# Kernel tuning notes

Hardware: AMD Instinct MI355X
Metric: run time of the kernel (lower is better)

The kernel has to match this reference:

```python
import jax, jax.numpy as jnp
import numpy as np

S, B, H = 2048, 2, 4096
NH, NG, HD = 32, 2, 128        # query heads, kv groups, head dim
ROT = 64                        # rotary dims (half of head dim)


def apply_rope(x, rope):
    # x: [s, b, n, hd]; rope: [s, 1, rot//2, 2]
    s = x.shape[0]
    rot = rope.shape[-2] * 2
    xr, xp = x[..., :rot], x[..., rot:]
    xs = xr.reshape(xr.shape[:-1] + (rot // 2, 2))          # [s,b,n,rot/2,2]
    rc = rope[:s].reshape(s, 1, 1, rot // 2, 2)             # broadcast over b, n
    c, sn = rc[..., 0], rc[..., 1]
    x0, x1 = xs[..., 0], xs[..., 1]
    out = jnp.stack([x0 * c - x1 * sn, x1 * c + x0 * sn], axis=-1)
    return jnp.concatenate([out.reshape(xr.shape), xp], axis=-1)


def setup_inputs() -> dict:
    key = jax.random.key(0)
    k1, k2, k3, k4 = jax.random.split(key, 4)
    hidden_states = jax.random.normal(k1, (S, B, H), dtype=jnp.float32)
    # causal boolean mask: True = attend
    causal = jnp.tril(jnp.ones((S, S), dtype=bool))
    attention_mask = jnp.broadcast_to(causal[None, None], (B, 1, S, S))
    # standard RoPE cache: [s, 1, rot//2, 2] = (cos, sin)
    pos = jnp.arange(S, dtype=jnp.float32)
    inv_freq = 1.0 / (10000.0 ** (jnp.arange(0, ROT // 2, dtype=jnp.float32) / (ROT // 2)))
    ang = pos[:, None] * inv_freq[None, :]
    rotary_pos_emb = jnp.stack([jnp.cos(ang), jnp.sin(ang)], axis=-1)[:, None]
    W_qkv = jax.random.normal(k2, (NH * HD + 2 * NG * HD, H), dtype=jnp.float32) * (H ** -0.5)
    b_qkv = jax.random.normal(k3, (NH * HD + 2 * NG * HD,), dtype=jnp.float32) * 0.02
    W_dense = jax.random.normal(k4, (H, NH * HD), dtype=jnp.float32) * ((NH * HD) ** -0.5)
    return {"hidden_states": hidden_states, "attention_mask": attention_mask,
            "rotary_pos_emb": rotary_pos_emb, "W_qkv": W_qkv, "b_qkv": b_qkv,
            "W_dense": W_dense}


def reference(hidden_states, attention_mask, rotary_pos_emb, W_qkv, b_qkv, W_dense):
    s, b, _ = hidden_states.shape
    r = NH // NG  # query heads per kv group
    mixed = jnp.einsum('sbh,oh->sbo', hidden_states, W_qkv) + b_qkv
    q = mixed[..., :NH * HD].reshape(s, b, NH, HD)
    k = mixed[..., NH * HD:NH * HD + NG * HD].reshape(s, b, NG, HD)
    v = mixed[..., NH * HD + NG * HD:].reshape(s, b, NG, HD)
    q = apply_rope(q, rotary_pos_emb)
    k = apply_rope(k, rotary_pos_emb)
    # GQA: keep kv at NG heads, give q a [g, r] split instead of materializing repeats
    qg = q.reshape(s, b, NG, r, HD)
    scale = HD ** -0.5
    scores = jnp.einsum('sbgrd,tbgd->bgrst', qg, k) * scale     # [b,g,r,s,t]
    mask = attention_mask[:, :, None]                            # [b,1,1,s,t]
    scores = jnp.where(mask, scores, jnp.finfo(scores.dtype).min)
    probs = jax.nn.softmax(scores, axis=-1)
    ctx = jnp.einsum('bgrst,tbgd->sbgrd', probs, v)              # [s,b,g,r,d]
    ctx = ctx.reshape(s, b, NH * HD)
    out = jnp.einsum('sbp,hp->sbh', ctx, W_dense)
    return out
```

## Files before the change

kernel.cpp:

```cpp
#include <hip/hip_runtime.h>
#include <cstdint>
#include <cstddef>


#define S_LEN 2048
#define BATCH 2
#define NHEADS 32
#define NGROUPS 2
#define HEADDIM 128
#define OQKV 4608
#define KSTRIDE 160
#define VSTRIDE 2080

typedef __attribute__((ext_vector_type(4))) float f32x4;
typedef __attribute__((ext_vector_type(4))) unsigned int u32x4;
typedef __attribute__((ext_vector_type(8))) unsigned short u16x8;
typedef __attribute__((ext_vector_type(8))) short s16x8;

union B8 { u32x4 q; u16x8 u; s16x8 s; };

__device__ __forceinline__ unsigned short f2b(float f) {
  unsigned int u = __builtin_bit_cast(unsigned int, f);
  u += 0x7fffu + ((u >> 16) & 1u);
  return (unsigned short)(u >> 16);
}
__device__ __forceinline__ float b2f(unsigned short h) {
  unsigned int u = ((unsigned int)h) << 16;
  return __builtin_bit_cast(float, u);
}

__device__ __forceinline__ void gload16(const unsigned short* g, unsigned short* l) {
  __builtin_amdgcn_global_load_lds(
      (const __attribute__((address_space(1))) void*)g,
      (__attribute__((address_space(3))) void*)l, 16, 0, 0);
}

__global__ __launch_bounds__(256) void cvt_kernel(const float* __restrict__ in,
                                                  unsigned short* __restrict__ out) {
  size_t i = (size_t)blockIdx.x * 256 + threadIdx.x;
  const f32x4* p = (const f32x4*)(in + i * 8);
  f32x4 a = p[0], b = p[1];
  B8 r;
  r.u[0] = f2b(a[0]); r.u[1] = f2b(a[1]); r.u[2] = f2b(a[2]); r.u[3] = f2b(a[3]);
  r.u[4] = f2b(b[0]); r.u[5] = f2b(b[1]); r.u[6] = f2b(b[2]); r.u[7] = f2b(b[3]);
  *(u32x4*)(out + i * 8) = r.q;
}

template<int A_FP32, int HAS_BIAS, int OUT_BF16>
__global__ __launch_bounds__(256) void gemm_bt(const void* __restrict__ Ap,
                                               const unsigned short* __restrict__ Bt,
                                               const float* __restrict__ bias,
                                               void* __restrict__ Cp,
                                               int M, int N, int K) {
  __shared__ __align__(16) unsigned short lA[128 * 32];
  __shared__ __align__(16) unsigned short lB[128 * 32];
  const int tid = threadIdx.x;
  const int wave = tid >> 6, lane = tid & 63;
  const int quad = lane >> 4, l15 = lane & 15;
  const int nwg = gridDim.x * gridDim.y;
  int lin = blockIdx.y * gridDim.x + blockIdx.x;
  int swz = (lin & 7) * (nwg >> 3) + (lin >> 3);
  const int bx = swz % gridDim.x, by = swz / gridDim.x;
  const int m0 = by * 128, n0 = bx * 128;
  const int wm = (wave & 1) * 64, wn = (wave >> 1) * 64;
  const int grow = wave * 16 + (lane >> 2);
  const int gcol = (lane & 3) * 8;
  unsigned short* lAw = lA + wave * 512;
  unsigned short* lBw = lB + wave * 512;
  f32x4 acc[4][4] = {};
  const unsigned short* Ab = (const unsigned short*)Ap;
  const float* Af = (const float*)Ap;
  const int ar = tid >> 1, acf = (tid & 1) * 16;
  f32x4 x0, x1, x2, x3;
  if (A_FP32) {
    const f32x4* p = (const f32x4*)(Af + (size_t)(m0 + ar) * K + acf);
    x0 = p[0]; x1 = p[1]; x2 = p[2]; x3 = p[3];
  }
  for (int k0 = 0; k0 < K; k0 += 32) {
    __syncthreads();
    if (A_FP32) {
      B8 c0, c1;
      for (int e = 0; e < 4; ++e) {
        c0.u[e] = f2b(x0[e]); c0.u[e + 4] = f2b(x1[e]);
        c1.u[e] = f2b(x2[e]); c1.u[e + 4] = f2b(x3[e]);
      }
      *(u32x4*)(lA + ar * 32 + acf) = c0.q;
      *(u32x4*)(lA + ar * 32 + acf + 8) = c1.q;
    } else {
      gload16(Ab + (size_t)(m0 + grow) * K + k0 + gcol, lAw);
      gload16(Ab + (size_t)(m0 + 64 + grow) * K + k0 + gcol, lAw + 2048);
    }
    gload16(Bt + (size_t)(n0 + grow) * K + k0 + gcol, lBw);
    gload16(Bt + (size_t)(n0 + 64 + grow) * K + k0 + gcol, lBw + 2048);
    __syncthreads();
    if (A_FP32 && k0 + 32 < K) {
      const f32x4* p = (const f32x4*)(Af + (size_t)(m0 + ar) * K + k0 + 32 + acf);
      x0 = p[0]; x1 = p[1]; x2 = p[2]; x3 = p[3];
    }
    B8 af[4], bf[4];
    for (int i = 0; i < 4; ++i)
      af[i].q = *(const u32x4*)(lA + (wm + 16 * i + l15) * 32 + quad * 8);
    for (int j = 0; j < 4; ++j)
      bf[j].q = *(const u32x4*)(lB + (wn + 16 * j + l15) * 32 + quad * 8);
    for (int i = 0; i < 4; ++i)
      for (int j = 0; j < 4; ++j)
        acc[i][j] = __builtin_amdgcn_mfma_f32_16x16x32_bf16(af[i].s, bf[j].s, acc[i][j], 0, 0, 0);
  }
  for (int i = 0; i < 4; ++i) {
    int gm = m0 + wm + 16 * i + quad * 4;
    for (int j = 0; j < 4; ++j) {
      int gn = n0 + wn + 16 * j + l15;
      float bb = HAS_BIAS ? bias[gn] : 0.0f;
      for (int r = 0; r < 4; ++r) {
        float v = acc[i][j][r] + bb;
        if (OUT_BF16)
          ((unsigned short*)Cp)[(size_t)(gm + r) * N + gn] = f2b(v);
        else
          ((float*)Cp)[(size_t)(gm + r) * N + gn] = v;
      }
    }
  }
}

__global__ __launch_bounds__(256) void rope_scatter(const unsigned short* __restrict__ mixed,
                                                    const float* __restrict__ rope,
                                                    unsigned short* __restrict__ qb,
                                                    unsigned short* __restrict__ kb,
                                                    unsigned short* __restrict__ vt) {
  unsigned int idx = blockIdx.x * 256 + threadIdx.x;
  unsigned int row = idx / 2304;
  unsigned int pr = idx - row * 2304;
  unsigned int o = pr * 2;
  unsigned int s = row >> 1, b = row & 1;
  unsigned int pq = *(const unsigned int*)(mixed + (size_t)row * OQKV + o);
  float x0 = b2f((unsigned short)(pq & 0xffff));
  float x1 = b2f((unsigned short)(pq >> 16));
  if (o >= 4352) {
    unsigned int g = (o - 4352) >> 7;
    unsigned int d = (o - 4352) & 127;
    unsigned short* base = vt + ((size_t)(b * NGROUPS + g) * HEADDIM + d) * VSTRIDE + s;
    base[0] = f2b(x0);
    base[VSTRIDE] = f2b(x1);
    return;
  }
  unsigned short* dst;
  unsigned int d;
  bool is_q = (o < 4096);
  if (is_q) {
    unsigned int h = o >> 7; d = o & 127;
    dst = qb + (((size_t)(b * NHEADS + h) * S_LEN + s) * HEADDIM + d);
  } else {
    unsigned int g = (o - 4096) >> 7; d = (o - 4096) & 127;
    dst = kb + (((size_t)(b * NGROUPS + g) * S_LEN + s) * KSTRIDE + d);
  }
  if (d < 64) {
    unsigned int i = d >> 1;
    float c = rope[s * 64 + i * 2], sn = rope[s * 64 + i * 2 + 1];
    float y0 = x0 * c - x1 * sn;
    float y1 = x1 * c + x0 * sn;
    x0 = y0; x1 = y1;
  }
  if (is_q) {
    const float scale = 0.08838834764831845f;
    x0 *= scale; x1 *= scale;
  }
  dst[0] = f2b(x0);
  dst[1] = f2b(x1);
}

__global__ __launch_bounds__(256) void attn_kernel(const unsigned short* __restrict__ qb,
                                                   const unsigned short* __restrict__ kb,
                                                   const unsigned short* __restrict__ vt,
                                                   unsigned short* __restrict__ ctx) {
  __shared__ __align__(16) unsigned short lk[64 * 128];
  __shared__ __align__(16) unsigned short lv[128 * 64];
  __shared__ __align__(16) unsigned short lp[4][16 * 72];
  const int qt = 31 - blockIdx.x;
  const int h = blockIdx.y, b = blockIdx.z;
  const int g = h >> 4;
  const int tid = threadIdx.x;
  const int wave = tid >> 6, lane = tid & 63;
  const int quad = lane >> 4, l15 = lane & 15;
  const int q0 = qt * 64 + wave * 16;
  unsigned short* lpw = lp[wave];
  char* lkb = (char*)lk;
  char* lvb = (char*)lv;

  const unsigned short* qp =
      qb + ((size_t)(b * NHEADS + h) * S_LEN + q0 + l15) * HEADDIM + quad * 8;
  B8 aq[4];
  for (int c = 0; c < 4; ++c) aq[c].q = *(const u32x4*)(qp + 32 * c);

  const unsigned short* kbase = kb + (size_t)(b * NGROUPS + g) * S_LEN * KSTRIDE;
  const unsigned short* vbase = vt + (size_t)(b * NGROUPS + g) * HEADDIM * VSTRIDE;

  const int krow = tid >> 2, kcol = (tid & 3) * 32;
  const int vrow = tid >> 1, vcol = (tid & 1) * 32;
  const int kxs = (krow & 7) << 4, vxs = (vrow & 7) << 4;
  const int kwb = krow * 256 + kcol * 2;
  const int vwb = vrow * 128 + vcol * 2;

  f32x4 o[8] = {};
  float lrow[4] = {0.f, 0.f, 0.f, 0.f};

  B8 kR0, kR1, kR2, kR3, vR0, vR1, vR2, vR3;
  {
    const unsigned short* kg = kbase + (size_t)krow * KSTRIDE + kcol;
    const unsigned short* vg = vbase + (size_t)vrow * VSTRIDE + vcol;
    kR0.q = *(const u32x4*)(kg);      kR1.q = *(const u32x4*)(kg + 8);
    kR2.q = *(const u32x4*)(kg + 16); kR3.q = *(const u32x4*)(kg + 24);
    vR0.q = *(const u32x4*)(vg);      vR1.q = *(const u32x4*)(vg + 8);
    vR2.q = *(const u32x4*)(vg + 16); vR3.q = *(const u32x4*)(vg + 24);
  }

  for (int kt = 0; kt <= qt; ++kt) {
    const int k0 = kt * 64;
    __syncthreads();
    *(u32x4*)(lkb + ((kwb +  0) ^ kxs)) = kR0.q;
    *(u32x4*)(lkb + ((kwb + 16) ^ kxs)) = kR1.q;
    *(u32x4*)(lkb + ((kwb + 32) ^ kxs)) = kR2.q;
    *(u32x4*)(lkb + ((kwb + 48) ^ kxs)) = kR3.q;
    *(u32x4*)(lvb + ((vwb +  0) ^ vxs)) = vR0.q;
    *(u32x4*)(lvb + ((vwb + 16) ^ vxs)) = vR1.q;
    *(u32x4*)(lvb + ((vwb + 32) ^ vxs)) = vR2.q;
    *(u32x4*)(lvb + ((vwb + 48) ^ vxs)) = vR3.q;
    __syncthreads();
    if (kt < qt) {
      const int k1 = k0 + 64;
      const unsigned short* kg = kbase + (size_t)(k1 + krow) * KSTRIDE + kcol;
      const unsigned short* vg = vbase + (size_t)vrow * VSTRIDE + k1 + vcol;
      kR0.q = *(const u32x4*)(kg);      kR1.q = *(const u32x4*)(kg + 8);
      kR2.q = *(const u32x4*)(kg + 16); kR3.q = *(const u32x4*)(kg + 24);
      vR0.q = *(const u32x4*)(vg);      vR1.q = *(const u32x4*)(vg + 8);
      vR2.q = *(const u32x4*)(vg + 16); vR3.q = *(const u32x4*)(vg + 24);
    }
    f32x4 sfr[4] = {};
    for (int t = 0; t < 4; ++t) {
      const int row = 16 * t + l15;
      const int rxs = (row & 7) << 4;
      const int rb = row * 256 + quad * 16;
      for (int c = 0; c < 4; ++c) {
        B8 bk;
        bk.q = *(const u32x4*)(lkb + ((rb + 64 * c) ^ rxs));
        sfr[t] = __builtin_amdgcn_mfma_f32_16x16x32_bf16(aq[c].s, bk.s, sfr[t], 0, 0, 0);
      }
    }
    const bool masked = (kt == qt);
    for (int r = 0; r < 4; ++r) {
      const int qq = q0 + quad * 4 + r;
      float psum = 0.f;
      for (int t = 0; t < 4; ++t) {
        float p = __expf(sfr[t][r]);
        if (masked && (k0 + 16 * t + l15 > qq)) p = 0.f;
        psum += p;
        lpw[(quad * 4 + r) * 72 + 16 * t + l15] = f2b(p);
      }
      lrow[r] += psum;
    }
    B8 pa0, pa1;
    pa0.q = *(const u32x4*)(lpw + l15 * 72 + quad * 8);
    pa1.q = *(const u32x4*)(lpw + l15 * 72 + 32 + quad * 8);
    for (int j = 0; j < 8; ++j) {
      const int row = 16 * j + l15;
      const int rxs = (row & 7) << 4;
      const int rb = row * 128 + quad * 16;
      B8 b0, b1;
      b0.q = *(const u32x4*)(lvb + (rb ^ rxs));
      b1.q = *(const u32x4*)(lvb + ((rb + 64) ^ rxs));
      o[j] = __builtin_amdgcn_mfma_f32_16x16x32_bf16(pa0.s, b0.s, o[j], 0, 0, 0);
      o[j] = __builtin_amdgcn_mfma_f32_16x16x32_bf16(pa1.s, b1.s, o[j], 0, 0, 0);
    }
  }
  float inv[4];
  for (int r = 0; r < 4; ++r) {
    float l = lrow[r];
    l += __shfl_xor(l, 1);
    l += __shfl_xor(l, 2);
    l += __shfl_xor(l, 4);
    l += __shfl_xor(l, 8);
    inv[r] = 1.0f / l;
  }
  for (int j = 0; j < 8; ++j) {
    for (int r = 0; r < 4; ++r) {
      int s = q0 + quad * 4 + r;
      ctx[(size_t)(s * BATCH + b) * 4096 + (size_t)h * HEADDIM + 16 * j + l15] =
          f2b(o[j][r] * inv[r]);
    }
  }
}

extern "C" void kernel_launch(void* const* d_in, const int* in_sizes, int n_in,
                              void* d_out, int out_size, void* d_ws, size_t ws_size,
                              hipStream_t stream) {
  const float* hidden = (const float*)d_in[0];
  const float* rope = (const float*)d_in[2];
  const float* Wqkv = (const float*)d_in[3];
  const float* bqkv = (const float*)d_in[4];
  const float* Wdense = (const float*)d_in[5];
  float* out = (float*)d_out;
  char* ws = (char*)d_ws;

  unsigned short* Wqkv_b   = (unsigned short*)(ws);
  unsigned short* Wdense_b = (unsigned short*)(ws + 37748736);
  unsigned short* mixedb   = (unsigned short*)(ws + 71303168);
  unsigned short* vtbuf    = (unsigned short*)(ws + 109051904);
  unsigned short* qbuf     = (unsigned short*)(ws);
  unsigned short* kbuf     = (unsigned short*)(ws + 33554432);
  unsigned short* ctxb     = (unsigned short*)(ws + 71303168);

  cvt_kernel<<<9216, 256, 0, stream>>>(Wqkv, Wqkv_b);
  cvt_kernel<<<8192, 256, 0, stream>>>(Wdense, Wdense_b);

  gemm_bt<1, 1, 1><<<dim3(36, 32), 256, 0, stream>>>(hidden, Wqkv_b, bqkv, mixedb,
                                                     4096, 4608, 4096);
  rope_scatter<<<36864, 256, 0, stream>>>(mixedb, rope, qbuf, kbuf, vtbuf);
  attn_kernel<<<dim3(32, 32, 2), 256, 0, stream>>>(qbuf, kbuf, vtbuf, ctxb);
  gemm_bt<0, 0, 0><<<dim3(32, 32), 256, 0, stream>>>(ctxb, Wdense_b, nullptr, out,
                                                     4096, 4096, 4096);
}
```

Baseline: 989.8 us.

## Replace GEMMs with 256x256 double-buffered swizzled-LDS kernel, pre-convert hidden to bf16

Both projection GEMMs now use a 512-thread kernel with 256x256 output tiles, LDS double buffering that prefetches the next K slice during MFMA work, and an XOR swizzle on LDS columns to avoid bank conflicts. The fp32 A-path is dropped: hidden states are converted to bf16 by a separate cvt pass into the output buffer, which serves as scratch until the final GEMM overwrites it. The larger tiles raise data reuse and halve the syncs per step, at the cost of more registers and LDS per block and fewer blocks than there are CUs (288 and 256).

Result: faster. 964.3 us (-2.6%).

```diff
diff --git a/kernel.cpp b/kernel.cpp
--- a/kernel.cpp
+++ b/kernel.cpp
@@ -46,71 +46,78 @@
   *(u32x4*)(out + i * 8) = r.q;
 }
 
-template<int A_FP32, int HAS_BIAS, int OUT_BF16>
-__global__ __launch_bounds__(256) void gemm_bt(const void* __restrict__ Ap,
+template<int HAS_BIAS, int OUT_BF16>
+__global__ __launch_bounds__(512) void gemm256(const unsigned short* __restrict__ Ab,
                                                const unsigned short* __restrict__ Bt,
                                                const float* __restrict__ bias,
                                                void* __restrict__ Cp,
                                                int M, int N, int K) {
-  __shared__ __align__(16) unsigned short lA[128 * 32];
-  __shared__ __align__(16) unsigned short lB[128 * 32];
+  __shared__ __align__(16) unsigned short lA[2][256 * 32];
+  __shared__ __align__(16) unsigned short lB[2][256 * 32];
   const int tid = threadIdx.x;
   const int wave = tid >> 6, lane = tid & 63;
   const int quad = lane >> 4, l15 = lane & 15;
+  const int wm = (wave >> 2) * 128;
+  const int wn = (wave & 3) * 64;
   const int nwg = gridDim.x * gridDim.y;
   int lin = blockIdx.y * gridDim.x + blockIdx.x;
   int swz = (lin & 7) * (nwg >> 3) + (lin >> 3);
   const int bx = swz % gridDim.x, by = swz / gridDim.x;
-  const int m0 = by * 128, n0 = bx * 128;
-  const int wm = (wave & 1) * 64, wn = (wave >> 1) * 64;
-  const int grow = wave * 16 + (lane >> 2);
-  const int gcol = (lane & 3) * 8;
-  unsigned short* lAw = lA + wave * 512;
-  unsigned short* lBw = lB + wave * 512;
-  f32x4 acc[4][4] = {};
-  const unsigned short* Ab = (const unsigned short*)Ap;
-  const float* Af = (const float*)Ap;
-  const int ar = tid >> 1, acf = (tid & 1) * 16;
-  f32x4 x0, x1, x2, x3;
-  if (A_FP32) {
-    const f32x4* p = (const f32x4*)(Af + (size_t)(m0 + ar) * K + acf);
-    x0 = p[0]; x1 = p[1]; x2 = p[2]; x3 = p[3];
-  }
-  for (int k0 = 0; k0 < K; k0 += 32) {
-    __syncthreads();
-    if (A_FP32) {
-      B8 c0, c1;
-      for (int e = 0; e < 4; ++e) {
-        c0.u[e] = f2b(x0[e]); c0.u[e + 4] = f2b(x1[e]);
-        c1.u[e] = f2b(x2[e]); c1.u[e + 4] = f2b(x3[e]);
-      }
-      *(u32x4*)(lA + ar * 32 + acf) = c0.q;
-      *(u32x4*)(lA + ar * 32 + acf + 8) = c1.q;
-    } else {
-      gload16(Ab + (size_t)(m0 + grow) * K + k0 + gcol, lAw);
-      gload16(Ab + (size_t)(m0 + 64 + grow) * K + k0 + gcol, lAw + 2048);
-    }
-    gload16(Bt + (size_t)(n0 + grow) * K + k0 + gcol, lBw);
-    gload16(Bt + (size_t)(n0 + 64 + grow) * K + k0 + gcol, lBw + 2048);
-    __syncthreads();
-    if (A_FP32 && k0 + 32 < K) {
-      const f32x4* p = (const f32x4*)(Af + (size_t)(m0 + ar) * K + k0 + 32 + acf);
-      x0 = p[0]; x1 = p[1]; x2 = p[2]; x3 = p[3];
-    }
-    B8 af[4], bf[4];
-    for (int i = 0; i < 4; ++i)
-      af[i].q = *(const u32x4*)(lA + (wm + 16 * i + l15) * 32 + quad * 8);
+  const int m0 = by * 256, n0 = bx * 256;
+  const int sr0 = wave * 32;
+  const int lrow = lane >> 2;
+  const int xcol = ((lane & 3) ^ (lrow & 3)) * 8;
+  const int fcol = (quad ^ (l15 & 3)) * 8;
+  f32x4 acc[8][4] = {};
+  const int nt = K >> 5;
+  int cur = 0;
+
+  {
+    const unsigned short* Ag = Ab + (size_t)(m0 + sr0 + lrow) * K + xcol;
+    const unsigned short* Bg = Bt + (size_t)(n0 + sr0 + lrow) * K + xcol;
+    gload16(Ag, lA[0] + sr0 * 32);
+    gload16(Ag + (size_t)16 * K, lA[0] + (sr0 + 16) * 32);
+    gload16(Bg, lB[0] + sr0 * 32);
+    gload16(Bg + (size_t)16 * K, lB[0] + (sr0 + 16) * 32);
+  }
+  __syncthreads();
+
+  for (int t = 0; t < nt; ++t) {
+    if (t + 1 < nt) {
+      const int kk = (t + 1) << 5;
+      const unsigned short* Ag = Ab + (size_t)(m0 + sr0 + lrow) * K + kk + xcol;
+      const unsigned short* Bg = Bt + (size_t)(n0 + sr0 + lrow) * K + kk + xcol;
+      unsigned short* dA = lA[cur ^ 1] + sr0 * 32;
+      unsigned short* dB = lB[cur ^ 1] + sr0 * 32;
+      gload16(Ag, dA);
+      gload16(Ag + (size_t)16 * K, dA + 512);
+      gload16(Bg, dB);
+      gload16(Bg + (size_t)16 * K, dB + 512);
+    }
+    B8 af[8], bf[4];
+#pragma unroll
+    for (int i = 0; i < 8; ++i)
+      af[i].q = *(const u32x4*)(lA[cur] + (wm + 16 * i + l15) * 32 + fcol);
+#pragma unroll
     for (int j = 0; j < 4; ++j)
-      bf[j].q = *(const u32x4*)(lB + (wn + 16 * j + l15) * 32 + quad * 8);
-    for (int i = 0; i < 4; ++i)
+      bf[j].q = *(const u32x4*)(lB[cur] + (wn + 16 * j + l15) * 32 + fcol);
+#pragma unroll
+    for (int i = 0; i < 8; ++i)
+#pragma unroll
       for (int j = 0; j < 4; ++j)
         acc[i][j] = __builtin_amdgcn_mfma_f32_16x16x32_bf16(af[i].s, bf[j].s, acc[i][j], 0, 0, 0);
-  }
-  for (int i = 0; i < 4; ++i) {
+    __syncthreads();
+    cur ^= 1;
+  }
+
+#pragma unroll
+  for (int i = 0; i < 8; ++i) {
     int gm = m0 + wm + 16 * i + quad * 4;
+#pragma unroll
     for (int j = 0; j < 4; ++j) {
       int gn = n0 + wn + 16 * j + l15;
       float bb = HAS_BIAS ? bias[gn] : 0.0f;
+#pragma unroll
       for (int r = 0; r < 4; ++r) {
         float v = acc[i][j][r] + bb;
         if (OUT_BF16)
@@ -307,14 +314,16 @@
   unsigned short* qbuf     = (unsigned short*)(ws);
   unsigned short* kbuf     = (unsigned short*)(ws + 33554432);
   unsigned short* ctxb     = (unsigned short*)(ws + 71303168);
+  unsigned short* hidden_b = (unsigned short*)d_out;
 
   cvt_kernel<<<9216, 256, 0, stream>>>(Wqkv, Wqkv_b);
   cvt_kernel<<<8192, 256, 0, stream>>>(Wdense, Wdense_b);
-
-  gemm_bt<1, 1, 1><<<dim3(36, 32), 256, 0, stream>>>(hidden, Wqkv_b, bqkv, mixedb,
-                                                     4096, 4608, 4096);
+  cvt_kernel<<<8192, 256, 0, stream>>>(hidden, hidden_b);
+
+  gemm256<1, 1><<<dim3(18, 16), 512, 0, stream>>>(hidden_b, Wqkv_b, bqkv, mixedb,
+                                                  4096, 4608, 4096);
   rope_scatter<<<36864, 256, 0, stream>>>(mixedb, rope, qbuf, kbuf, vtbuf);
   attn_kernel<<<dim3(32, 32, 2), 256, 0, stream>>>(qbuf, kbuf, vtbuf, ctxb);
-  gemm_bt<0, 0, 0><<<dim3(32, 32), 256, 0, stream>>>(ctxb, Wdense_b, nullptr, out,
-                                                     4096, 4096, 4096);
-}
+  gemm256<0, 0><<<dim3(16, 16), 512, 0, stream>>>(ctxb, Wdense_b, nullptr, out,
+                                                  4096, 4096, 4096);
+}
```
